# Kernel tuning notes

Hardware: AMD Instinct MI355X
Metric: run time of the kernel (lower is better)

## Reference

```python
import jax, jax.numpy as jnp
import numpy as np

B, N, T, N_IN = 4, 40, 64, 4
N_EMB, N_HID = 32, 64
EPS = 1e-05


def _spatial_rels(n):
    # fully-connected directed edges without self-loops (NRI convention)
    offdiag = np.ones((n, n)) - np.eye(n)
    recv_idx, send_idx = np.where(offdiag)[0], np.where(offdiag)[1]
    eye = np.eye(n, dtype=np.float32)
    return eye[recv_idx], eye[send_idx]  # [n*(n-1), n] each


def _temporal_rels(t):
    # all t*t ordered pairs (including self), one-hot
    eye = np.eye(t, dtype=np.float32)
    recv = np.repeat(np.arange(t), t)
    send = np.tile(np.arange(t), t)
    return eye[recv], eye[send]  # [t*t, t] each


def setup_inputs() -> dict:
    key = jax.random.key(0)
    ks = jax.random.split(key, 8)
    rel_rec, rel_send = _spatial_rels(N)
    rel_rec_t, rel_send_t = _temporal_rels(T)
    s_emb = 1.0 / np.sqrt(N_IN)
    s_lstm = 1.0 / np.sqrt(N_HID)
    s_att = 1.0 / np.sqrt(2 * N_HID)
    return {
        "inputs": jax.random.normal(ks[0], (B, N, T, N_IN), dtype=jnp.float32),
        "rel_rec": jnp.asarray(rel_rec),
        "rel_send": jnp.asarray(rel_send),
        "rel_rec_t": jnp.asarray(rel_rec_t),
        "rel_send_t": jnp.asarray(rel_send_t),
        "W_emb": jax.random.uniform(ks[1], (N_EMB, N_IN), jnp.float32, -s_emb, s_emb),
        "b_emb": jnp.zeros((N_EMB,), jnp.float32),
        "W_ih": jax.random.uniform(ks[2], (4 * N_HID, N_EMB), jnp.float32, -s_lstm, s_lstm),
        "W_hh": jax.random.uniform(ks[3], (4 * N_HID, N_HID), jnp.float32, -s_lstm, s_lstm),
        "b_ih": jax.random.uniform(ks[4], (4 * N_HID,), jnp.float32, -s_lstm, s_lstm),
        "b_hh": jax.random.uniform(ks[5], (4 * N_HID,), jnp.float32, -s_lstm, s_lstm),
        "W_att": jax.random.uniform(ks[6], (1, 2 * N_HID), jnp.float32, -s_att, s_att),
        "b_att": jnp.zeros((1,), jnp.float32),
    }


def _forward(inputs, rel_rec, rel_send, rel_rec_t, rel_send_t,
             W_emb, b_emb, W_ih, W_hh, b_ih, b_hh, W_att, b_att):
    b, n, t, _ = inputs.shape
    nh = W_hh.shape[1]
    locs = inputs[..., :2]

    # ---- LSTMEncoder: per-timestep embedding + LSTM cell (scan over time) ----
    emb = jnp.einsum("bnti,ei->bnte", inputs, W_emb) + b_emb       # [B,N,T,n_emb]
    xs = emb.transpose(2, 0, 1, 3).reshape(t, b * n, -1)            # [T,BN,n_emb]

    def step(carry, x):
        h, c = carry
        gates = x @ W_ih.T + b_ih + h @ W_hh.T + b_hh               # [BN,4H]
        i_g, f_g, g_g, o_g = jnp.split(gates, 4, axis=-1)           # torch gate order i,f,g,o
        i_g = jax.nn.sigmoid(i_g)
        f_g = jax.nn.sigmoid(f_g)
        g_g = jnp.tanh(g_g)
        o_g = jax.nn.sigmoid(o_g)
        c = f_g * c + i_g * g_g
        h = o_g * jnp.tanh(c)
        return (h, c), h

    h0 = jnp.zeros((b * n, nh), inputs.dtype)
    _, hs_t = jax.lax.scan(step, (h0, h0), xs)                      # [T,BN,H]
    hs = hs_t.transpose(1, 0, 2).reshape(b, n, t, nh)               # [B,N,T,H]

    # ---- SoftAttention over timesteps ----
    hsf = hs.reshape(b * n, t, nh)                                  # [BN,T,H]
    senders = jnp.einsum("kt,mth->mkh", rel_send_t, hsf)            # [BN,T*T,H]
    receivers = jnp.einsum("kt,mth->mkh", rel_rec_t, hsf)
    edges = jnp.concatenate([senders, receivers], axis=-1)          # [BN,T*T,2H]
    scores = jnp.einsum("mkf,of->mko", edges, W_att)[..., 0] + b_att[0]  # [BN,T*T]
    # adj = rel_send_t^T @ diag(scores) @ rel_rec_t (done without diag_embed)
    adj_s = jnp.einsum("ki,mk,kj->mij", rel_send_t, scores, rel_rec_t)   # [BN,T,T]
    adj_sn = jax.nn.softmax(adj_s, axis=-1)
    cs = jnp.einsum("mij,mjh->mih", adj_sn, hsf).reshape(b, n, t, nh)    # [B,N,T,H]

    # ---- HardwiredAttention over atoms ----
    locs_re = locs.reshape(b, n, -1)                                 # [B,N,T*2]
    snd = jnp.einsum("en,bnf->bef", rel_send, locs_re).reshape(b, -1, t, 2)
    rcv = jnp.einsum("en,bnf->bef", rel_rec, locs_re).reshape(b, -1, t, 2)
    dist = jnp.sqrt(((snd - rcv) ** 2).sum(-1))                      # [B,E,T]
    w = (1.0 / (dist + EPS)).transpose(0, 2, 1)                      # [B,T,E]
    adj_h = jnp.einsum("ei,bte,ej->btij", rel_send, w, rel_rec)      # [B,T,N,N]
    ch = jnp.einsum("btij,btjh->btih", adj_h, hs.transpose(0, 2, 1, 3))
    ch = ch.transpose(0, 2, 1, 3)                                    # [B,N,T,H]

    c_out = jnp.tanh(jnp.concatenate([cs[:, :, -1, :], ch.sum(2)], axis=-1))  # [B,N,2H]
    return c_out


def reference(inputs, rel_rec, rel_send, rel_rec_t, rel_send_t,
              W_emb, b_emb, W_ih, W_hh, b_ih, b_hh, W_att, b_att):
    return _forward(inputs, rel_rec, rel_send, rel_rec_t, rel_send_t,
                    W_emb, b_emb, W_ih, W_hh, b_ih, b_hh, W_att, b_att)
```

## Files before the change

### kernel.cpp

```cpp
#include <hip/hip_runtime.h>
#include <math.h>

#define BB   4
#define NN   40
#define TT   64
#define NIN  4
#define NEMB 32
#define NHID 64
#define NG   256
#define EPSW 1e-5f

__device__ __align__(16) float g_hs[BB * NN * TT * NHID];

__device__ __forceinline__ float fast_sigmoid(float x) {
    return __fdividef(1.0f, 1.0f + __expf(-x));
}
__device__ __forceinline__ float fast_tanh(float x) {
    return __fdividef(2.0f, 1.0f + __expf(-2.0f * x)) - 1.0f;
}
__device__ __forceinline__ float lanebcast(float v, int l) {
    return __int_as_float(__builtin_amdgcn_readlane(__float_as_int(v), l));
}

__global__ __launch_bounds__(256, 1)
void k_lstm(const float* __restrict__ inputs,
            const float* __restrict__ W_emb,
            const float* __restrict__ b_emb,
            const float* __restrict__ W_ih,
            const float* __restrict__ W_hh,
            const float* __restrict__ b_ih,
            const float* __restrict__ b_hh,
            const float* __restrict__ W_att,
            float* __restrict__ out)
{
    __shared__ __align__(16) float s_x[TT * NIN];
    __shared__ __align__(16) float s_act[2][NG];
    __shared__ __align__(16) float s_hs[TT * (NHID + 1)];
    __shared__ __align__(16) float s_war[NHID];
    __shared__ __align__(16) float s_p[TT];

    const int m   = blockIdx.x;
    const int tid = threadIdx.x;
    const int g   = tid;
    const int j   = tid & 63;
    const int gtype = g >> 6;

    s_x[tid] = inputs[m * (TT * NIN) + tid];
    if (tid < NHID) s_war[tid] = W_att[NHID + tid];

    const float* rowp = W_hh + g * NHID;
    float4 w0, w1, w2, w3, w4, w5, w6, w7, w8, w9, wA, wB, wC, wD, wE, wF;
    #define ALOAD(W, OFF) asm volatile( \
        "global_load_dwordx4 %0, %1, off offset:" #OFF : "=v"(W) : "v"(rowp))
    ALOAD(w0, 0);    ALOAD(w1, 16);   ALOAD(w2, 32);   ALOAD(w3, 48);
    ALOAD(w4, 64);   ALOAD(w5, 80);   ALOAD(w6, 96);   ALOAD(w7, 112);
    ALOAD(w8, 128);  ALOAD(w9, 144);  ALOAD(wA, 160);  ALOAD(wB, 176);
    ALOAD(wC, 192);  ALOAD(wD, 208);  ALOAD(wE, 224);  ALOAD(wF, 240);
    #undef ALOAD
    asm volatile("s_waitcnt vmcnt(0)" ::: "memory");
    __builtin_amdgcn_sched_barrier(0);

    float wcx = 0.f, wcy = 0.f, wcz = 0.f, wcw = 0.f;
    float bc  = b_ih[g] + b_hh[g];
    {
        const float4* wih4  = (const float4*)(W_ih + g * NEMB);
        const float4* wemb4 = (const float4*)W_emb;
        #pragma unroll
        for (int e4 = 0; e4 < NEMB / 4; ++e4) {
            float4 wv = wih4[e4];
            float4 m0 = wemb4[4 * e4 + 0];
            float4 m1 = wemb4[4 * e4 + 1];
            float4 m2 = wemb4[4 * e4 + 2];
            float4 m3 = wemb4[4 * e4 + 3];
            wcx += wv.x * m0.x + wv.y * m1.x + wv.z * m2.x + wv.w * m3.x;
            wcy += wv.x * m0.y + wv.y * m1.y + wv.z * m2.y + wv.w * m3.y;
            wcz += wv.x * m0.z + wv.y * m1.z + wv.z * m2.z + wv.w * m3.z;
            wcw += wv.x * m0.w + wv.y * m1.w + wv.z * m2.w + wv.w * m3.w;
            bc  += wv.x * b_emb[4 * e4 + 0] + wv.y * b_emb[4 * e4 + 1]
                 + wv.z * b_emb[4 * e4 + 2] + wv.w * b_emb[4 * e4 + 3];
        }
    }

    __syncthreads();

    float c = 0.0f, h = 0.0f;
    #pragma unroll 1
    for (int t = 0; t < TT; ++t) {
        const int p = t & 1;
        const float4 x = ((const float4*)s_x)[t];

        float v0 = bc, v1 = 0.f, v2 = 0.f, v3 = 0.f;
        #define DOT4(W, K) {                                  \
            v0 += lanebcast(h, 4*(K)+0) * W.x;                \
            v1 += lanebcast(h, 4*(K)+1) * W.y;                \
            v2 += lanebcast(h, 4*(K)+2) * W.z;                \
            v3 += lanebcast(h, 4*(K)+3) * W.w; }
        DOT4(w0, 0)  DOT4(w1, 1)  DOT4(w2, 2)  DOT4(w3, 3)
        DOT4(w4, 4)  DOT4(w5, 5)  DOT4(w6, 6)  DOT4(w7, 7)
        DOT4(w8, 8)  DOT4(w9, 9)  DOT4(wA, 10) DOT4(wB, 11)
        DOT4(wC, 12) DOT4(wD, 13) DOT4(wE, 14) DOT4(wF, 15)
        #undef DOT4
        const float vx = x.x * wcx + x.y * wcy + x.z * wcz + x.w * wcw;
        const float v  = ((v0 + v1) + (v2 + v3)) + vx;

        const float a = (gtype == 2) ? fast_tanh(v) : fast_sigmoid(v);
        s_act[p][g] = a;
        __syncthreads();

        const float ig = s_act[p][j];
        const float fg = s_act[p][NHID + j];
        const float gg = s_act[p][2 * NHID + j];
        const float og = s_act[p][3 * NHID + j];
        c = fg * c + ig * gg;
        h = og * fast_tanh(c);
        if (gtype == 0) s_hs[t * (NHID + 1) + j] = h;
    }
    __syncthreads();

    #pragma unroll
    for (int idx = tid; idx < TT * NHID; idx += 256) {
        const int t = idx >> 6, hh = idx & 63;
        g_hs[m * (TT * NHID) + idx] = s_hs[t * (NHID + 1) + hh];
    }

    if (tid < TT) {
        const int t = tid;
        float r = 0.0f;
        #pragma unroll
        for (int k = 0; k < NHID; ++k)
            r += s_hs[t * (NHID + 1) + k] * s_war[k];
        float mx = r;
        #pragma unroll
        for (int off = 32; off >= 1; off >>= 1)
            mx = fmaxf(mx, __shfl_xor(mx, off));
        const float e = __expf(r - mx);
        float s = e;
        #pragma unroll
        for (int off = 32; off >= 1; off >>= 1)
            s += __shfl_xor(s, off);
        s_p[t] = __fdividef(e, s);
    }
    __syncthreads();

    if (tid < NHID) {
        float acc = 0.0f;
        #pragma unroll
        for (int t = 0; t < TT; ++t)
            acc += s_p[t] * s_hs[t * (NHID + 1) + tid];
        out[m * (2 * NHID) + tid] = fast_tanh(acc);
    }
}

__global__ __launch_bounds__(1024)
void k_spatial(const float* __restrict__ inputs,
               float* __restrict__ out)
{
    __shared__ float s_w[TT * NN];
    __shared__ float s_part[16 * NHID];

    const int bi  = blockIdx.x;
    const int b   = bi / NN;
    const int i   = bi - b * NN;
    const int tid = threadIdx.x;

    for (int idx = tid; idx < TT * NN; idx += 1024) {
        const int t = idx / NN;
        const int j = idx - t * NN;
        const float* pi = inputs + ((b * NN + i) * TT + t) * NIN;
        const float* pj = inputs + ((b * NN + j) * TT + t) * NIN;
        const float dx = pi[0] - pj[0];
        const float dy = pi[1] - pj[1];
        const float d  = sqrtf(dx * dx + dy * dy);
        s_w[idx] = (j == i) ? 0.0f : __fdividef(1.0f, d + EPSW);
    }
    __syncthreads();

    const int h = tid & 63;
    const int q = tid >> 6;

    const float* base = g_hs + (size_t)b * NN * TT * NHID + h;
    float a0 = 0.f, a1 = 0.f, a2 = 0.f, a3 = 0.f;
    for (int t = q * 4; t < q * 4 + 4; ++t) {
        const float* hp = base + t * NHID;
        const float* wp = s_w + t * NN;
        #pragma unroll
        for (int j = 0; j < NN; j += 4) {
            a0 += wp[j + 0] * hp[(size_t)(j + 0) * TT * NHID];
            a1 += wp[j + 1] * hp[(size_t)(j + 1) * TT * NHID];
            a2 += wp[j + 2] * hp[(size_t)(j + 2) * TT * NHID];
            a3 += wp[j + 3] * hp[(size_t)(j + 3) * TT * NHID];
        }
    }
    s_part[q * NHID + h] = (a0 + a1) + (a2 + a3);
    __syncthreads();

    if (tid < NHID) {
        float s = 0.f;
        #pragma unroll
        for (int q2 = 0; q2 < 16; ++q2)
            s += s_part[q2 * NHID + tid];
        out[bi * (2 * NHID) + NHID + tid] = fast_tanh(s);
    }
}

extern "C" void kernel_launch(void* const* d_in, const int* in_sizes, int n_in,
                              void* d_out, int out_size, void* d_ws, size_t ws_size,
                              hipStream_t stream) {
    const float* inputs = (const float*)d_in[0];
    const float* W_emb  = (const float*)d_in[5];
    const float* b_emb  = (const float*)d_in[6];
    const float* W_ih   = (const float*)d_in[7];
    const float* W_hh   = (const float*)d_in[8];
    const float* b_ih   = (const float*)d_in[9];
    const float* b_hh   = (const float*)d_in[10];
    const float* W_att  = (const float*)d_in[11];
    (void)d_ws; (void)ws_size;

    float* outp = (float*)d_out;

    hipLaunchKernelGGL(k_lstm, dim3(BB * NN), dim3(256), 0, stream,
                       inputs, W_emb, b_emb, W_ih, W_hh, b_ih, b_hh, W_att,
                       outp);
    hipLaunchKernelGGL(k_spatial, dim3(BB * NN), dim3(1024), 0, stream,
                       inputs, outp);
}
```

Before: 142.8 us.

## Split LSTM recurrent dot product across two thread halves per block

Doubles the LSTM block to 512 threads and has each half compute a 32-element slice of the W_hh row dot product. The partial sums go to shared memory, and every thread adds the two halves and applies the gate nonlinearities itself. This shortens the serial per-timestep FMA/readlane chain on the critical recurrence path and halves the weight registers per thread. In exchange it adds shared-memory traffic and redundant activation work, and the barrier each step now spans 8 waves.

```diff
diff --git a/kernel.cpp b/kernel.cpp
--- a/kernel.cpp
+++ b/kernel.cpp
@@ -22,7 +22,7 @@
     return __int_as_float(__builtin_amdgcn_readlane(__float_as_int(v), l));
 }
 
-__global__ __launch_bounds__(256, 1)
+__global__ __launch_bounds__(512, 1)
 void k_lstm(const float* __restrict__ inputs,
             const float* __restrict__ W_emb,
             const float* __restrict__ b_emb,
@@ -34,31 +34,19 @@
             float* __restrict__ out)
 {
     __shared__ __align__(16) float s_x[TT * NIN];
-    __shared__ __align__(16) float s_act[2][NG];
+    __shared__ __align__(16) float s_part[2][2][NG];
     __shared__ __align__(16) float s_hs[TT * (NHID + 1)];
     __shared__ __align__(16) float s_war[NHID];
     __shared__ __align__(16) float s_p[TT];
 
-    const int m   = blockIdx.x;
-    const int tid = threadIdx.x;
-    const int g   = tid;
-    const int j   = tid & 63;
-    const int gtype = g >> 6;
-
-    s_x[tid] = inputs[m * (TT * NIN) + tid];
-    if (tid < NHID) s_war[tid] = W_att[NHID + tid];
-
-    const float* rowp = W_hh + g * NHID;
-    float4 w0, w1, w2, w3, w4, w5, w6, w7, w8, w9, wA, wB, wC, wD, wE, wF;
-    #define ALOAD(W, OFF) asm volatile( \
-        "global_load_dwordx4 %0, %1, off offset:" #OFF : "=v"(W) : "v"(rowp))
-    ALOAD(w0, 0);    ALOAD(w1, 16);   ALOAD(w2, 32);   ALOAD(w3, 48);
-    ALOAD(w4, 64);   ALOAD(w5, 80);   ALOAD(w6, 96);   ALOAD(w7, 112);
-    ALOAD(w8, 128);  ALOAD(w9, 144);  ALOAD(wA, 160);  ALOAD(wB, 176);
-    ALOAD(wC, 192);  ALOAD(wD, 208);  ALOAD(wE, 224);  ALOAD(wF, 240);
-    #undef ALOAD
-    asm volatile("s_waitcnt vmcnt(0)" ::: "memory");
-    __builtin_amdgcn_sched_barrier(0);
+    const int m    = blockIdx.x;
+    const int tid  = threadIdx.x;
+    const int half = tid >> 8;
+    const int g    = tid & 255;
+    const int j    = tid & 63;
+
+    if (tid < TT * NIN) s_x[tid] = inputs[m * (TT * NIN) + tid];
+    if (tid < NHID)     s_war[tid] = W_att[NHID + tid];
 
     float wcx = 0.f, wcy = 0.f, wcz = 0.f, wcw = 0.f;
     float bc  = b_ih[g] + b_hh[g];
@@ -80,6 +68,13 @@
                  + wv.z * b_emb[4 * e4 + 2] + wv.w * b_emb[4 * e4 + 3];
         }
     }
+    if (half) { wcx = wcy = wcz = wcw = 0.f; bc = 0.f; }
+
+    const float4* q4 = (const float4*)(W_hh + g * NHID + half * 32);
+    float4 w0 = q4[0], w1 = q4[1], w2 = q4[2], w3 = q4[3];
+    float4 w4 = q4[4], w5 = q4[5], w6 = q4[6], w7 = q4[7];
+
+    const int kb = half * 32;
 
     __syncthreads();
 
@@ -91,34 +86,35 @@
 
         float v0 = bc, v1 = 0.f, v2 = 0.f, v3 = 0.f;
         #define DOT4(W, K) {                                  \
-            v0 += lanebcast(h, 4*(K)+0) * W.x;                \
-            v1 += lanebcast(h, 4*(K)+1) * W.y;                \
-            v2 += lanebcast(h, 4*(K)+2) * W.z;                \
-            v3 += lanebcast(h, 4*(K)+3) * W.w; }
+            v0 += lanebcast(h, kb + 4*(K)+0) * W.x;           \
+            v1 += lanebcast(h, kb + 4*(K)+1) * W.y;           \
+            v2 += lanebcast(h, kb + 4*(K)+2) * W.z;           \
+            v3 += lanebcast(h, kb + 4*(K)+3) * W.w; }
         DOT4(w0, 0)  DOT4(w1, 1)  DOT4(w2, 2)  DOT4(w3, 3)
         DOT4(w4, 4)  DOT4(w5, 5)  DOT4(w6, 6)  DOT4(w7, 7)
-        DOT4(w8, 8)  DOT4(w9, 9)  DOT4(wA, 10) DOT4(wB, 11)
-        DOT4(wC, 12) DOT4(wD, 13) DOT4(wE, 14) DOT4(wF, 15)
         #undef DOT4
         const float vx = x.x * wcx + x.y * wcy + x.z * wcz + x.w * wcw;
         const float v  = ((v0 + v1) + (v2 + v3)) + vx;
 
-        const float a = (gtype == 2) ? fast_tanh(v) : fast_sigmoid(v);
-        s_act[p][g] = a;
+        s_part[p][half][g] = v;
         __syncthreads();
 
-        const float ig = s_act[p][j];
-        const float fg = s_act[p][NHID + j];
-        const float gg = s_act[p][2 * NHID + j];
-        const float og = s_act[p][3 * NHID + j];
+        const float iv = s_part[p][0][          j] + s_part[p][1][          j];
+        const float fv = s_part[p][0][NHID   + j] + s_part[p][1][NHID   + j];
+        const float gv = s_part[p][0][2*NHID + j] + s_part[p][1][2*NHID + j];
+        const float ov = s_part[p][0][3*NHID + j] + s_part[p][1][3*NHID + j];
+        const float ig = fast_sigmoid(iv);
+        const float fg = fast_sigmoid(fv);
+        const float gg = fast_tanh(gv);
+        const float og = fast_sigmoid(ov);
         c = fg * c + ig * gg;
         h = og * fast_tanh(c);
-        if (gtype == 0) s_hs[t * (NHID + 1) + j] = h;
+        if (tid < 64) s_hs[t * (NHID + 1) + j] = h;
     }
     __syncthreads();
 
     #pragma unroll
-    for (int idx = tid; idx < TT * NHID; idx += 256) {
+    for (int idx = tid; idx < TT * NHID; idx += 512) {
         const int t = idx >> 6, hh = idx & 63;
         g_hs[m * (TT * NHID) + idx] = s_hs[t * (NHID + 1) + hh];
     }
@@ -218,7 +214,7 @@
 
     float* outp = (float*)d_out;
 
-    hipLaunchKernelGGL(k_lstm, dim3(BB * NN), dim3(256), 0, stream,
+    hipLaunchKernelGGL(k_lstm, dim3(BB * NN), dim3(512), 0, stream,
                        inputs, W_emb, b_emb, W_ih, W_hh, b_ih, b_hh, W_att,
                        outp);
     hipLaunchKernelGGL(k_spatial, dim3(BB * NN), dim3(1024), 0, stream,
```

After: 163.1 us. +14.3%, slower.
